# Optimization experiments

Hardware: AMD Instinct MI355X
Metric: run time of the kernel (lower is better)

## Reference

```python
import jax, jax.numpy as jnp
import numpy as np

D_MODEL = 1024
N_HEADS = 16
HEAD = D_MODEL // N_HEADS
B, S = 2, 2048


def setup_inputs() -> dict:
    key = jax.random.key(0)
    ks = jax.random.split(key, 9)
    sc = 1.0 / np.sqrt(D_MODEL)
    return {
        "q": jax.random.normal(ks[0], (B, S, D_MODEL), dtype=jnp.float32),
        "k": jax.random.normal(ks[1], (B, S, D_MODEL), dtype=jnp.float32),
        "v": jax.random.normal(ks[2], (B, S, D_MODEL), dtype=jnp.float32),
        "mask": jnp.zeros((S, S), dtype=jnp.float32),
        "Wq": jax.random.normal(ks[3], (D_MODEL, D_MODEL), dtype=jnp.float32) * sc,
        "bq": jnp.zeros((D_MODEL,), dtype=jnp.float32),
        "Wk": jax.random.normal(ks[4], (D_MODEL, D_MODEL), dtype=jnp.float32) * sc,
        "bk": jnp.zeros((D_MODEL,), dtype=jnp.float32),
        "Wv": jax.random.normal(ks[5], (D_MODEL, D_MODEL), dtype=jnp.float32) * sc,
        "bv": jnpp_zeros() if False else jnp.zeros((D_MODEL,), dtype=jnp.float32),
    }


def reference(q, k, v, mask, Wq, bq, Wk, bk, Wv, bv):
    # Linear projections (torch Linear: x @ W.T + b)
    qp = q @ Wq.T + bq  # (B, S, D)
    kp = k @ Wk.T + bk
    vp = v @ Wv.T + bv
    # split heads -> (B, H, S, Hd)
    def split(x):
        return x.reshape(B, S, N_HEADS, HEAD).transpose(0, 2, 1, 3)
    qh, kh, vh = split(qp), split(kp), split(vp)
    scores = jnp.einsum('bhqd,bhkd->bhqk', qh, kh) / np.sqrt(HEAD)
    scores = scores + mask  # additive mask broadcast over (B, H)
    attn = jax.nn.softmax(scores, axis=-1)
    out = jnp.einsum('bhqk,bhkd->bhqd', attn, vh)
    return out.transpose(0, 2, 1, 3).reshape(B, S, D_MODEL)
```

## Files before the change

kernel.cpp:

```cpp
#include <hip/hip_runtime.h>
#include <cstdint>

#define DM 1024
#define NH 16
#define HDIM 64
#define SEQ 2048
#define NB 2
#define L2E 1.44269504f

typedef unsigned short u16;
typedef unsigned int u32;
typedef __attribute__((ext_vector_type(8))) short bf16x8;
typedef __attribute__((ext_vector_type(8))) unsigned short u16x8;
typedef __attribute__((ext_vector_type(4))) unsigned int u32x4;
typedef __attribute__((ext_vector_type(4))) float f32x4;
typedef __attribute__((ext_vector_type(16))) float f32x16;
typedef __attribute__((ext_vector_type(4))) unsigned short u16x4;

__device__ __forceinline__ u16 f2bf(float f) {
  uint32_t x = __float_as_uint(f);
  x += 0x7fffu + ((x >> 16) & 1u);
  return (u16)(x >> 16);
}

__device__ __forceinline__ u32 pack_bf2t(float lo, float hi) {
  return __builtin_amdgcn_perm(__float_as_uint(hi), __float_as_uint(lo), 0x07060302u);
}

__device__ __forceinline__ void gload_lds16(const void* g, void* lds) {
  __builtin_amdgcn_global_load_lds(
      (const __attribute__((address_space(1))) unsigned int*)(uintptr_t)g,
      (__attribute__((address_space(3))) unsigned int*)(uint32_t)(uintptr_t)lds,
      16, 0, 0);
}


__global__ __launch_bounds__(256) void cvt_kernel(
    const float4* __restrict__ s0, const float4* __restrict__ s1, const float4* __restrict__ s2,
    const float4* __restrict__ s3, const float4* __restrict__ s4, const float4* __restrict__ s5,
    u16x4* __restrict__ d0, u16x4* __restrict__ d1, u16x4* __restrict__ d2,
    u16x4* __restrict__ d3, u16x4* __restrict__ d4, u16x4* __restrict__ d5) {
  int i = blockIdx.x * 256 + threadIdx.x;
  const float4* s;
  u16x4* d;
  int off;
  if (i < 3 * 1048576) {
    int seg = i >> 20;
    off = i & 1048575;
    s = seg == 0 ? s0 : (seg == 1 ? s1 : s2);
    d = seg == 0 ? d0 : (seg == 1 ? d1 : d2);
  } else {
    int j = i - 3 * 1048576;
    int seg = j >> 18;
    off = j & 262143;
    s = seg == 0 ? s3 : (seg == 1 ? s4 : s5);
    d = seg == 0 ? d3 : (seg == 1 ? d4 : d5);
  }
  float4 v = s[off];
  u16x4 o = {f2bf(v.x), f2bf(v.y), f2bf(v.z), f2bf(v.w)};
  d[off] = o;
}

__global__ __launch_bounds__(256) void maskprep_kernel(const float* __restrict__ mask,
                                                       u16* __restrict__ maskP) {
  __shared__ float tile[32][257];
  const int t = threadIdx.x;
  const int q0 = blockIdx.x * 32;
#pragma unroll
  for (int ss = 0; ss < 2; ++ss) {
    const int st = blockIdx.y * 2 + ss;
    const int kv0 = st * 256;
    if (ss) __syncthreads();
#pragma unroll
    for (int p = 0; p < 8; ++p) {
      const int row = p * 4 + (t >> 6);
      const int col = (t & 63) * 4;
      *(float4*)&tile[row][col] = *(const float4*)&mask[(size_t)(q0 + row) * SEQ + kv0 + col];
    }
    __syncthreads();
    const int tgl = t >> 5, ql = t & 31;
    u16 outv[32];
#pragma unroll
    for (int i = 0; i < 32; ++i) {
      const int hl = i >> 4, r = i & 15;
      const int kvl = (r & 3) + 8 * (r >> 2) + 4 * hl;
      outv[i] = f2bf(tile[ql][tgl * 32 + kvl] * L2E);
    }
    u16* dst = maskP + ((size_t)(st * 8 + tgl) * SEQ + (q0 + ql)) * 32;
#pragma unroll
    for (int j = 0; j < 4; ++j) *(u16x8*)(dst + 8 * j) = *(const u16x8*)&outv[8 * j];
  }
}

__global__ __launch_bounds__(256) void proj_kernel(
    const u16* __restrict__ Xq, const u16* __restrict__ Xk, const u16* __restrict__ Xv,
    const u16* __restrict__ Wqp, const u16* __restrict__ Wkp, const u16* __restrict__ Wvp,
    const float* __restrict__ bqp, const float* __restrict__ bkp, const float* __restrict__ bvp,
    u16* __restrict__ Qp, u16* __restrict__ Kp, u16* __restrict__ Vt) {
  __shared__ __align__(16) u16 sA[2][128 * 32];
  __shared__ __align__(16) u16 sB[2][128 * 32];
  const int t = threadIdx.x;
  const int w = t >> 6, lane = t & 63, quad = lane >> 4, l16 = lane & 15;
  const int wr = w >> 1, wc = w & 1;
  const int hw = blockIdx.x + (blockIdx.y << 3) + (blockIdx.z << 8);
  const int logical = (hw & 7) * 96 + (hw >> 3);
  const int bx = logical & 7, by = (logical >> 3) & 31, bz = logical >> 8;
  const int m0 = by * 128, n0 = bx * 128;
  const int mode = bz;
  const u16* X = mode == 0 ? Xq : (mode == 1 ? Xk : Xv);
  const u16* W = mode == 0 ? Wqp : (mode == 1 ? Wkp : Wvp);
  const float* bias = mode == 0 ? bqp : (mode == 1 ? bkp : bvp);

  f32x4 acc[4][4] = {};
  const int srow = lane >> 2;
  const int scol = (lane & 3) * 16;

#pragma unroll
  for (int j = 0; j < 2; ++j) {
    const int rbase = (w * 2 + j) * 16;
    gload_lds16((const char*)X + ((size_t)(m0 + rbase + srow) * DM) * 2 + scol,
                (char*)sA[0] + rbase * 64);
    gload_lds16((const char*)W + ((size_t)(n0 + rbase + srow) * DM) * 2 + scol,
                (char*)sB[0] + rbase * 64);
  }

  for (int it = 0; it < 32; ++it) {
    const int p = it & 1;
    __syncthreads();
    if (it < 31) {
      const int k0 = (it + 1) * 32;
#pragma unroll
      for (int j = 0; j < 2; ++j) {
        const int rbase = (w * 2 + j) * 16;
        gload_lds16((const char*)X + ((size_t)(m0 + rbase + srow) * DM + k0) * 2 + scol,
                    (char*)sA[p ^ 1] + rbase * 64);
        gload_lds16((const char*)W + ((size_t)(n0 + rbase + srow) * DM + k0) * 2 + scol,
                    (char*)sB[p ^ 1] + rbase * 64);
      }
    }
    bf16x8 af[4], bfr[4];
#pragma unroll
    for (int i = 0; i < 4; ++i)
      af[i] = *(const bf16x8*)&sA[p][(wr * 64 + i * 16 + l16) * 32 + quad * 8];
#pragma unroll
    for (int j = 0; j < 4; ++j)
      bfr[j] = *(const bf16x8*)&sB[p][(wc * 64 + j * 16 + l16) * 32 + quad * 8];
#pragma unroll
    for (int i = 0; i < 4; ++i)
#pragma unroll
      for (int j = 0; j < 4; ++j)
        acc[i][j] = __builtin_amdgcn_mfma_f32_16x16x32_bf16(af[i], bfr[j], acc[i][j], 0, 0, 0);
  }

  float bb[4];
#pragma unroll
  for (int j = 0; j < 4; ++j) bb[j] = bias[n0 + wc * 64 + j * 16 + l16];
  const float scl = (mode == 0) ? 0.18033688011f : 1.0f;

#pragma unroll
  for (int i = 0; i < 4; ++i) {
    const int mbase = m0 + wr * 64 + i * 16 + quad * 4;
    const int bidx = mbase >> 11;
    const int s = mbase & 2047;
#pragma unroll
    for (int j = 0; j < 4; ++j) {
      const int n = n0 + wc * 64 + j * 16 + l16;
      const int h = n >> 6, hd = n & 63;
      const size_t hb = (size_t)(bidx * NH + h) * (SEQ * HDIM);
      if (mode == 2) {
        const int tv = (s >> 5) * 2048 + (hd >> 5) * 1024 + ((s >> 4) & 1) * 512 +
                       ((s >> 3) & 1) * 256 + (hd & 31) * 8 + (s & 7);
        u16x4 pk = {f2bf(acc[i][j][0] + bb[j]), f2bf(acc[i][j][1] + bb[j]),
                    f2bf(acc[i][j][2] + bb[j]), f2bf(acc[i][j][3] + bb[j])};
        *(u16x4*)&Vt[hb + tv] = pk;
      } else {
        u16* dst = (mode == 0) ? Qp : Kp;
        const int th = (s >> 5) * 2048 + (hd >> 4) * 512 + ((hd >> 3) & 1) * 256 +
                       (s & 31) * 8 + (hd & 7);
#pragma unroll
        for (int r = 0; r < 4; ++r)
          dst[hb + th + r * 8] = f2bf((acc[i][j][r] + bb[j]) * scl);
      }
    }
  }
}

__global__ __launch_bounds__(256, 2) void attn_kernel(
    const u16* __restrict__ Qp, const u16* __restrict__ Kp,
    const u16* __restrict__ Vt, const u16* __restrict__ maskP,
    float* __restrict__ out) {
  __shared__ float sO[4][32][65];
  __shared__ float sL[4][64];
  const int t = threadIdx.x, w = t >> 6, lane = t & 63;
  const int l31 = lane & 31, hl = lane >> 5;
  const int h = blockIdx.x, qt = blockIdx.y, b = blockIdx.z;
  const int q0 = qt * 64;
  const u16* Qh = Qp + (size_t)(b * NH + h) * (SEQ * HDIM);
  const u16* Kh = Kp + (size_t)(b * NH + h) * (SEQ * HDIM);
  const u16* Vh = Vt + (size_t)(b * NH + h) * (SEQ * HDIM);

  bf16x8 qf[2][4];
#pragma unroll
  for (int sub = 0; sub < 2; ++sub)
#pragma unroll
    for (int kt = 0; kt < 4; ++kt)
      qf[sub][kt] =
          *(const bf16x8*)(Qh + (size_t)((q0 >> 5) + sub) * 2048 + kt * 512 + lane * 8);

  const int Tb = w * 16;
  const u16* Kt = Kh + (size_t)Tb * 2048 + (size_t)lane * 8;
  const u16* Vw = Vh + (size_t)Tb * 2048 + (size_t)lane * 8;
  const u16* mb0 = maskP + ((size_t)Tb * SEQ + (q0 + l31)) * 32 + hl * 16;
  const u16* mb1 = mb0 + 32 * 32;

  f32x16 oacc[2][2] = {};
  float l_run[2] = {0.f, 0.f};

  bf16x8 kf[4], vf[2][2];
#pragma unroll
  for (int kt = 0; kt < 4; ++kt) kf[kt] = *(const bf16x8*)(Kt + kt * 512);
#pragma unroll
  for (int half = 0; half < 2; ++half)
#pragma unroll
    for (int ks = 0; ks < 2; ++ks)
      vf[half][ks] = *(const bf16x8*)(Vw + half * 1024 + ks * 512);
  u32x4 mk[2][2];
  mk[0][0] = *(const u32x4*)(mb0);
  mk[0][1] = *(const u32x4*)(mb0 + 8);
  mk[1][0] = *(const u32x4*)(mb1);
  mk[1][1] = *(const u32x4*)(mb1 + 8);

#pragma unroll 2
  for (int it = 0; it < 16; ++it) {
    const int itn = it < 15 ? it + 1 : 15;

    bf16x8 pfr[2][2];
#pragma unroll
    for (int sub = 0; sub < 2; ++sub) {
      f32x16 st;
#pragma unroll
      for (int r = 0; r < 8; ++r) {
        const u32 word = (r < 4 ? mk[sub][0][r & 3] : mk[sub][1][r & 3]);
        st[2 * r] = __uint_as_float(word << 16);
        st[2 * r + 1] = __uint_as_float(word & 0xffff0000u);
      }
      {
        const u16* mb = (sub ? mb1 : mb0) + (size_t)itn * (SEQ * 32);
        mk[sub][0] = *(const u32x4*)(mb);
        mk[sub][1] = *(const u32x4*)(mb + 8);
      }
#pragma unroll
      for (int kt = 0; kt < 4; ++kt)
        st = __builtin_amdgcn_mfma_f32_32x32x16_bf16(kf[kt], qf[sub][kt], st, 0, 0, 0);
      if (sub == 1) {
#pragma unroll
        for (int kt = 0; kt < 4; ++kt)
          kf[kt] = *(const bf16x8*)(Kt + (size_t)itn * 2048 + kt * 512);
      }

      float ls = 0.f;
#pragma unroll
      for (int r = 0; r < 16; ++r) {
        st[r] = __builtin_amdgcn_exp2f(st[r]);
        ls += st[r];
      }
      l_run[sub] += ls;

      u32 pk[4][2];
#pragma unroll
      for (int g = 0; g < 4; ++g) {
        pk[g][0] = pack_bf2t(st[4 * g + 0], st[4 * g + 1]);
        pk[g][1] = pack_bf2t(st[4 * g + 2], st[4 * g + 3]);
      }
#pragma unroll
      for (int ks = 0; ks < 2; ++ks) {
        u32 sa = hl ? pk[2 * ks][0] : pk[2 * ks + 1][0];
        u32 sb = hl ? pk[2 * ks][1] : pk[2 * ks + 1][1];
        u32 ra = __shfl_xor(sa, 32);
        u32 rb = __shfl_xor(sb, 32);
        u32 oa = hl ? pk[2 * ks + 1][0] : pk[2 * ks][0];
        u32 ob = hl ? pk[2 * ks + 1][1] : pk[2 * ks][1];
        union {
          u32 u[4];
          bf16x8 v;
        } f;
        f.u[0] = hl ? ra : oa;
        f.u[1] = hl ? rb : ob;
        f.u[2] = hl ? oa : ra;
        f.u[3] = hl ? ob : rb;
        pfr[sub][ks] = f.v;
      }
    }

#pragma unroll
    for (int sub = 0; sub < 2; ++sub)
#pragma unroll
      for (int ks = 0; ks < 2; ++ks) {
        oacc[0][sub] = __builtin_amdgcn_mfma_f32_32x32x16_bf16(vf[0][ks], pfr[sub][ks],
                                                               oacc[0][sub], 0, 0, 0);
        oacc[1][sub] = __builtin_amdgcn_mfma_f32_32x32x16_bf16(vf[1][ks], pfr[sub][ks],
                                                               oacc[1][sub], 0, 0, 0);
      }

#pragma unroll
    for (int half = 0; half < 2; ++half)
#pragma unroll
      for (int ks = 0; ks < 2; ++ks)
        vf[half][ks] =
            *(const bf16x8*)(Vw + (size_t)itn * 2048 + half * 1024 + ks * 512);
  }

  l_run[0] += __shfl_xor(l_run[0], 32);
  l_run[1] += __shfl_xor(l_run[1], 32);
  if (hl == 0) {
    sL[w][l31] = l_run[0];
    sL[w][32 + l31] = l_run[1];
  }

  const int hd = t & 31, grp = t >> 5;
#pragma unroll
  for (int half = 0; half < 2; ++half) {
    __syncthreads();
#pragma unroll
    for (int sub = 0; sub < 2; ++sub)
#pragma unroll
      for (int r = 0; r < 16; ++r)
        sO[w][(r & 3) + 8 * (r >> 2) + 4 * hl][sub * 32 + l31] = oacc[half][sub][r];
    __syncthreads();
#pragma unroll
    for (int p8 = 0; p8 < 8; ++p8) {
      const int qi = grp * 8 + p8;
      const float lsum = sL[0][qi] + sL[1][qi] + sL[2][qi] + sL[3][qi];
      const float val = sO[0][hd][qi] + sO[1][hd][qi] + sO[2][hd][qi] + sO[3][hd][qi];
      out[(size_t)(b * SEQ + q0 + qi) * DM + h * HDIM + half * 32 + hd] = val / lsum;
    }
  }
}

extern "C" void kernel_launch(void* const* d_in, const int* in_sizes, int n_in,
                              void* d_out, int out_size, void* d_ws, size_t ws_size,
                              hipStream_t stream) {
  const float* q = (const float*)d_in[0];
  const float* k = (const float*)d_in[1];
  const float* v = (const float*)d_in[2];
  const float* mask = (const float*)d_in[3];
  const float* Wq = (const float*)d_in[4];
  const float* bq = (const float*)d_in[5];
  const float* Wk = (const float*)d_in[6];
  const float* bk = (const float*)d_in[7];
  const float* Wv = (const float*)d_in[8];
  const float* bv = (const float*)d_in[9];

  char* ws = (char*)d_ws;
  u16* q_bf = (u16*)(ws + 0);
  u16* k_bf = (u16*)(ws + 8388608);
  u16* v_bf = (u16*)(ws + 16777216);
  u16* wq_bf = (u16*)(ws + 25165824);
  u16* wk_bf = (u16*)(ws + 27262976);
  u16* wv_bf = (u16*)(ws + 29360128);
  u16* Qp = (u16*)(ws + 31457280);
  u16* Kp = (u16*)(ws + 39845888);
  u16* Vt = (u16*)(ws + 48234496);
  u16* maskP = (u16*)(ws + 56623104);

  cvt_kernel<<<15360, 256, 0, stream>>>(
      (const float4*)q, (const float4*)k, (const float4*)v, (const float4*)Wq,
      (const float4*)Wk, (const float4*)Wv, (u16x4*)q_bf, (u16x4*)k_bf, (u16x4*)v_bf,
      (u16x4*)wq_bf, (u16x4*)wk_bf, (u16x4*)wv_bf);

  maskprep_kernel<<<dim3(64, 4), 256, 0, stream>>>(mask, maskP);

  proj_kernel<<<dim3(8, 32, 3), 256, 0, stream>>>(q_bf, k_bf, v_bf, wq_bf, wk_bf, wv_bf,
                                                  bq, bk, bv, Qp, Kp, Vt);

  attn_kernel<<<dim3(16, 32, 2), 256, 0, stream>>>(Qp, Kp, Vt, maskP, (float*)d_out);
}
```

Baseline: 219.8 us.

## Split attention queries across wave pairs using 512-thread blocks

Each attention block now runs 8 waves instead of 4, with each wave handling one 32-query subtile and a quarter of the keys, rather than both subtiles. This halves per-wave accumulators and serial work to improve latency hiding and occupancy. The cost is that K/V fragments are loaded twice (once per query subgroup) and the final cross-wave reduction spans more waves. Launch bounds change to 512 threads with 2 blocks per CU.

```diff
diff --git a/kernel.cpp b/kernel.cpp
--- a/kernel.cpp
+++ b/kernel.cpp
@@ -185,36 +185,33 @@
   }
 }
 
-__global__ __launch_bounds__(256, 2) void attn_kernel(
+__global__ __launch_bounds__(512, 2) void attn_kernel(
     const u16* __restrict__ Qp, const u16* __restrict__ Kp,
     const u16* __restrict__ Vt, const u16* __restrict__ maskP,
     float* __restrict__ out) {
-  __shared__ float sO[4][32][65];
-  __shared__ float sL[4][64];
+  __shared__ float sO[8][32][33];
+  __shared__ float sL[8][32];
   const int t = threadIdx.x, w = t >> 6, lane = t & 63;
   const int l31 = lane & 31, hl = lane >> 5;
   const int h = blockIdx.x, qt = blockIdx.y, b = blockIdx.z;
   const int q0 = qt * 64;
+  const int sub = w & 1, kg = w >> 1;
   const u16* Qh = Qp + (size_t)(b * NH + h) * (SEQ * HDIM);
   const u16* Kh = Kp + (size_t)(b * NH + h) * (SEQ * HDIM);
   const u16* Vh = Vt + (size_t)(b * NH + h) * (SEQ * HDIM);
 
-  bf16x8 qf[2][4];
-#pragma unroll
-  for (int sub = 0; sub < 2; ++sub)
-#pragma unroll
-    for (int kt = 0; kt < 4; ++kt)
-      qf[sub][kt] =
-          *(const bf16x8*)(Qh + (size_t)((q0 >> 5) + sub) * 2048 + kt * 512 + lane * 8);
-
-  const int Tb = w * 16;
+  bf16x8 qf[4];
+#pragma unroll
+  for (int kt = 0; kt < 4; ++kt)
+    qf[kt] = *(const bf16x8*)(Qh + (size_t)((q0 >> 5) + sub) * 2048 + kt * 512 + lane * 8);
+
+  const int Tb = kg * 16;
   const u16* Kt = Kh + (size_t)Tb * 2048 + (size_t)lane * 8;
   const u16* Vw = Vh + (size_t)Tb * 2048 + (size_t)lane * 8;
-  const u16* mb0 = maskP + ((size_t)Tb * SEQ + (q0 + l31)) * 32 + hl * 16;
-  const u16* mb1 = mb0 + 32 * 32;
-
-  f32x16 oacc[2][2] = {};
-  float l_run[2] = {0.f, 0.f};
+  const u16* mb = maskP + ((size_t)Tb * SEQ + (q0 + sub * 32 + l31)) * 32 + hl * 16;
+
+  f32x16 oacc[2] = {};
+  float l_run = 0.f;
 
   bf16x8 kf[4], vf[2][2];
 #pragma unroll
@@ -224,114 +221,94 @@
 #pragma unroll
     for (int ks = 0; ks < 2; ++ks)
       vf[half][ks] = *(const bf16x8*)(Vw + half * 1024 + ks * 512);
-  u32x4 mk[2][2];
-  mk[0][0] = *(const u32x4*)(mb0);
-  mk[0][1] = *(const u32x4*)(mb0 + 8);
-  mk[1][0] = *(const u32x4*)(mb1);
-  mk[1][1] = *(const u32x4*)(mb1 + 8);
+  u32x4 mk0 = *(const u32x4*)(mb);
+  u32x4 mk1 = *(const u32x4*)(mb + 8);
 
 #pragma unroll 2
   for (int it = 0; it < 16; ++it) {
     const int itn = it < 15 ? it + 1 : 15;
 
-    bf16x8 pfr[2][2];
-#pragma unroll
-    for (int sub = 0; sub < 2; ++sub) {
-      f32x16 st;
-#pragma unroll
-      for (int r = 0; r < 8; ++r) {
-        const u32 word = (r < 4 ? mk[sub][0][r & 3] : mk[sub][1][r & 3]);
-        st[2 * r] = __uint_as_float(word << 16);
-        st[2 * r + 1] = __uint_as_float(word & 0xffff0000u);
-      }
-      {
-        const u16* mb = (sub ? mb1 : mb0) + (size_t)itn * (SEQ * 32);
-        mk[sub][0] = *(const u32x4*)(mb);
-        mk[sub][1] = *(const u32x4*)(mb + 8);
-      }
-#pragma unroll
-      for (int kt = 0; kt < 4; ++kt)
-        st = __builtin_amdgcn_mfma_f32_32x32x16_bf16(kf[kt], qf[sub][kt], st, 0, 0, 0);
-      if (sub == 1) {
-#pragma unroll
-        for (int kt = 0; kt < 4; ++kt)
-          kf[kt] = *(const bf16x8*)(Kt + (size_t)itn * 2048 + kt * 512);
-      }
-
-      float ls = 0.f;
-#pragma unroll
-      for (int r = 0; r < 16; ++r) {
-        st[r] = __builtin_amdgcn_exp2f(st[r]);
-        ls += st[r];
-      }
-      l_run[sub] += ls;
-
-      u32 pk[4][2];
-#pragma unroll
-      for (int g = 0; g < 4; ++g) {
-        pk[g][0] = pack_bf2t(st[4 * g + 0], st[4 * g + 1]);
-        pk[g][1] = pack_bf2t(st[4 * g + 2], st[4 * g + 3]);
-      }
-#pragma unroll
-      for (int ks = 0; ks < 2; ++ks) {
-        u32 sa = hl ? pk[2 * ks][0] : pk[2 * ks + 1][0];
-        u32 sb = hl ? pk[2 * ks][1] : pk[2 * ks + 1][1];
-        u32 ra = __shfl_xor(sa, 32);
-        u32 rb = __shfl_xor(sb, 32);
-        u32 oa = hl ? pk[2 * ks + 1][0] : pk[2 * ks][0];
-        u32 ob = hl ? pk[2 * ks + 1][1] : pk[2 * ks][1];
-        union {
-          u32 u[4];
-          bf16x8 v;
-        } f;
-        f.u[0] = hl ? ra : oa;
-        f.u[1] = hl ? rb : ob;
-        f.u[2] = hl ? oa : ra;
-        f.u[3] = hl ? ob : rb;
-        pfr[sub][ks] = f.v;
-      }
-    }
-
-#pragma unroll
-    for (int sub = 0; sub < 2; ++sub)
-#pragma unroll
-      for (int ks = 0; ks < 2; ++ks) {
-        oacc[0][sub] = __builtin_amdgcn_mfma_f32_32x32x16_bf16(vf[0][ks], pfr[sub][ks],
-                                                               oacc[0][sub], 0, 0, 0);
-        oacc[1][sub] = __builtin_amdgcn_mfma_f32_32x32x16_bf16(vf[1][ks], pfr[sub][ks],
-                                                               oacc[1][sub], 0, 0, 0);
-      }
-
+    f32x16 st;
+#pragma unroll
+    for (int r = 0; r < 8; ++r) {
+      const u32 word = (r < 4 ? mk0[r & 3] : mk1[r & 3]);
+      st[2 * r] = __uint_as_float(word << 16);
+      st[2 * r + 1] = __uint_as_float(word & 0xffff0000u);
+    }
+    mk0 = *(const u32x4*)(mb + (size_t)itn * (SEQ * 32));
+    mk1 = *(const u32x4*)(mb + (size_t)itn * (SEQ * 32) + 8);
+
+#pragma unroll
+    for (int kt = 0; kt < 4; ++kt)
+      st = __builtin_amdgcn_mfma_f32_32x32x16_bf16(kf[kt], qf[kt], st, 0, 0, 0);
+#pragma unroll
+    for (int kt = 0; kt < 4; ++kt)
+      kf[kt] = *(const bf16x8*)(Kt + (size_t)itn * 2048 + kt * 512);
+
+    float ls = 0.f;
+#pragma unroll
+    for (int r = 0; r < 16; ++r) {
+      st[r] = __builtin_amdgcn_exp2f(st[r]);
+      ls += st[r];
+    }
+    l_run += ls;
+
+    u32 pk[4][2];
+#pragma unroll
+    for (int g = 0; g < 4; ++g) {
+      pk[g][0] = pack_bf2t(st[4 * g + 0], st[4 * g + 1]);
+      pk[g][1] = pack_bf2t(st[4 * g + 2], st[4 * g + 3]);
+    }
+    bf16x8 pfr[2];
+#pragma unroll
+    for (int ks = 0; ks < 2; ++ks) {
+      u32 sa = hl ? pk[2 * ks][0] : pk[2 * ks + 1][0];
+      u32 sb = hl ? pk[2 * ks][1] : pk[2 * ks + 1][1];
+      u32 ra = __shfl_xor(sa, 32);
+      u32 rb = __shfl_xor(sb, 32);
+      u32 oa = hl ? pk[2 * ks + 1][0] : pk[2 * ks][0];
+      u32 ob = hl ? pk[2 * ks + 1][1] : pk[2 * ks][1];
+      union {
+        u32 u[4];
+        bf16x8 v;
+      } f;
+      f.u[0] = hl ? ra : oa;
+      f.u[1] = hl ? rb : ob;
+      f.u[2] = hl ? oa : ra;
+      f.u[3] = hl ? ob : rb;
+      pfr[ks] = f.v;
+    }
+
+#pragma unroll
+    for (int ks = 0; ks < 2; ++ks) {
+      oacc[0] = __builtin_amdgcn_mfma_f32_32x32x16_bf16(vf[0][ks], pfr[ks], oacc[0], 0, 0, 0);
+      oacc[1] = __builtin_amdgcn_mfma_f32_32x32x16_bf16(vf[1][ks], pfr[ks], oacc[1], 0, 0, 0);
+    }
 #pragma unroll
     for (int half = 0; half < 2; ++half)
 #pragma unroll
       for (int ks = 0; ks < 2; ++ks)
-        vf[half][ks] =
-            *(const bf16x8*)(Vw + (size_t)itn * 2048 + half * 1024 + ks * 512);
-  }
-
-  l_run[0] += __shfl_xor(l_run[0], 32);
-  l_run[1] += __shfl_xor(l_run[1], 32);
-  if (hl == 0) {
-    sL[w][l31] = l_run[0];
-    sL[w][32 + l31] = l_run[1];
-  }
+        vf[half][ks] = *(const bf16x8*)(Vw + (size_t)itn * 2048 + half * 1024 + ks * 512);
+  }
+
+  l_run += __shfl_xor(l_run, 32);
+  if (hl == 0) sL[w][l31] = l_run;
 
   const int hd = t & 31, grp = t >> 5;
 #pragma unroll
   for (int half = 0; half < 2; ++half) {
     __syncthreads();
 #pragma unroll
-    for (int sub = 0; sub < 2; ++sub)
-#pragma unroll
-      for (int r = 0; r < 16; ++r)
-        sO[w][(r & 3) + 8 * (r >> 2) + 4 * hl][sub * 32 + l31] = oacc[half][sub][r];
+    for (int r = 0; r < 16; ++r)
+      sO[w][(r & 3) + 8 * (r >> 2) + 4 * hl][l31] = oacc[half][r];
     __syncthreads();
 #pragma unroll
-    for (int p8 = 0; p8 < 8; ++p8) {
-      const int qi = grp * 8 + p8;
-      const float lsum = sL[0][qi] + sL[1][qi] + sL[2][qi] + sL[3][qi];
-      const float val = sO[0][hd][qi] + sO[1][hd][qi] + sO[2][hd][qi] + sO[3][hd][qi];
+    for (int p4 = 0; p4 < 4; ++p4) {
+      const int qi = grp * 4 + p4;
+      const int qs = qi >> 5, qc = qi & 31;
+      const float lsum = sL[qs][qc] + sL[qs + 2][qc] + sL[qs + 4][qc] + sL[qs + 6][qc];
+      const float val = sO[qs][hd][qc] + sO[qs + 2][hd][qc] + sO[qs + 4][hd][qc] +
+                        sO[qs + 6][hd][qc];
       out[(size_t)(b * SEQ + q0 + qi) * DM + h * HDIM + half * 32 + hd] = val / lsum;
     }
   }
@@ -373,5 +350,5 @@
   proj_kernel<<<dim3(8, 32, 3), 256, 0, stream>>>(q_bf, k_bf, v_bf, wq_bf, wk_bf, wv_bf,
                                                   bq, bk, bv, Qp, Kp, Vt);
 
-  attn_kernel<<<dim3(16, 32, 2), 256, 0, stream>>>(Qp, Kp, Vt, maskP, (float*)d_out);
-}
+  attn_kernel<<<dim3(16, 32, 2), 512, 0, stream>>>(Qp, Kp, Vt, maskP, (float*)d_out);
+}
```

Measured after the change: 246.6 us. +12.2%, slower.
